# Kernel tuning notes

Measured on AMD Instinct MI355X. Metric: run time of the kernel, lower is better.

The kernel has to match this reference:

```python
import jax, jax.numpy as jnp
import numpy as np

KERNEL_SIZE = 5   # from __init__ default
SIGMA_S = 1.0     # spatial gaussian sigma (both axes)
SIGMA_R = 0.04    # range (color) gaussian sigma


def _space_kernel(k, sigma):
    # kornia-style 1D gaussian, normalized to sum 1, then outer product -> (k, k)
    x = jnp.arange(k, dtype=jnp.float32) - (k // 2)
    g = jnp.exp(-(x * x) / (2.0 * sigma * sigma))
    g = g / g.sum()
    return jnp.outer(g, g)


def setup_inputs() -> dict:
    key = jax.random.key(0)
    images = jax.random.uniform(key, (16, 512, 512, 3), dtype=jnp.float32)  # [B,H,W,3] in [0,1]
    return {"images": images}


def reference(images):
    k = KERNEL_SIZE
    pad = k // 2
    x = jnp.transpose(images, (0, 3, 1, 2))  # (B, C, H, W)
    B, C, H, W = x.shape
    xp = jnp.pad(x, ((0, 0), (0, 0), (pad, pad), (pad, pad)), mode="reflect")
    sk = _space_kernel(k, SIGMA_S).astype(x.dtype)
    inv2sr2 = 0.5 / (SIGMA_R * SIGMA_R)
    num = jnp.zeros_like(x)
    den = jnp.zeros((B, 1, H, W), dtype=x.dtype)
    # fused accumulation over the k*k window (fixed 25-tap loop, fully vectorized per tap)
    for dy in range(k):
        for dx in range(k):
            sh = xp[:, :, dy:dy + H, dx:dx + W]                  # shifted neighbor (B,C,H,W)
            d2 = jnp.sum((sh - x) ** 2, axis=1, keepdims=True)   # color distance^2 (B,1,H,W)
            w = sk[dy, dx] * jnp.exp(-inv2sr2 * d2)              # space * range weight
            num = num + w * sh
            den = den + w
    out = jnp.clip(num / den, 0.0, 1.0)
    return jnp.transpose(out, (0, 2, 3, 1))  # back to (B, H, W, C)
```

## Files before the change

kernel.cpp:

```cpp
#include <hip/hip_runtime.h>
#include <math.h>

#define IMG_H 512
#define IMG_W 512
#define CH    3
#define TILE_W 16
#define TILE_H 32
#define HALF  16
#define PAD   2
#define TP    20

typedef float v2f __attribute__((ext_vector_type(2)));
typedef float v4f __attribute__((ext_vector_type(4)));

#if __has_builtin(__builtin_amdgcn_exp2f)
#define EXP2(x) __builtin_amdgcn_exp2f(x)
#else
#define EXP2(x) exp2f(x)
#endif

#if __has_builtin(__builtin_amdgcn_rcpf)
#define RCP(x) __builtin_amdgcn_rcpf(x)
#else
#define RCP(x) (1.0f / (x))
#endif

__device__ __forceinline__ int reflect_idx(int i, int n) {
    i = (i < 0) ? -i : i;
    i = (i >= n) ? (2 * n - 2 - i) : i;
    return i;
}

__global__ __launch_bounds__(256)
void bilateral_kernel(const float* __restrict__ in, float* __restrict__ out) {
    __shared__ v4f planeP[TP][TP];
    __shared__ v4f planeQ[TP][TP];

    const float S = sqrtf(312.5f * 1.44269504088896f);

    const int b  = blockIdx.z;
    const int by = blockIdx.y * TILE_H;
    const int bx = blockIdx.x * TILE_W;
    const int tx = threadIdx.x;
    const int ty = threadIdx.y;
    const int tid = ty * TILE_W + tx;

    for (int i = tid; i < TP * TP; i += 256) {
        const int r  = i / TP;
        const int cc = i - r * TP;
        const int gyA = reflect_idx(by + r - PAD, IMG_H);
        const int gyB = reflect_idx(by + HALF + r - PAD, IMG_H);
        const int gx  = reflect_idx(bx + cc - PAD, IMG_W);
        const float* pA = in + ((size_t)(b * IMG_H + gyA) * IMG_W + gx) * CH;
        const float* pB = in + ((size_t)(b * IMG_H + gyB) * IMG_W + gx) * CH;
        const float a0 = pA[0] * S, a1 = pA[1] * S, a2 = pA[2] * S;
        const float e0 = pB[0] * S, e1 = pB[1] * S, e2 = pB[2] * S;
        const float wA = -fmaf(a0, a0, fmaf(a1, a1, a2 * a2));
        const float wB = -fmaf(e0, e0, fmaf(e1, e1, e2 * e2));
        planeP[r][cc] = (v4f){ a0, e0, a1, e1 };
        planeQ[r][cc] = (v4f){ a2, e2, wA, wB };
    }
    __syncthreads();

    const int rp = ((ty & 3) << 2) | (ty >> 2);

    const float CW[3] = { -4.1978935f, -2.0338538f, -1.3125121f };

    const v4f cP = planeP[rp + PAD][tx + PAD];
    const v4f cQ = planeQ[rp + PAD][tx + PAD];
    const v2f c2x = __builtin_shufflevector(cP, cP, 0, 1) + __builtin_shufflevector(cP, cP, 0, 1);
    const v2f c2y = __builtin_shufflevector(cP, cP, 2, 3) + __builtin_shufflevector(cP, cP, 2, 3);
    const v2f c2z = __builtin_shufflevector(cQ, cQ, 0, 1) + __builtin_shufflevector(cQ, cQ, 0, 1);
    const v2f cw  = __builtin_shufflevector(cQ, cQ, 2, 3);

    v2f base[3][3];
    #pragma unroll
    for (int iy = 0; iy < 3; ++iy)
        #pragma unroll
        for (int ix = 0; ix < 3; ++ix) {
            const float k = CW[iy] + CW[ix];
            base[iy][ix] = cw + (v2f){ k, k };
        }

    v2f nx = (v2f){0.f,0.f}, ny = (v2f){0.f,0.f};
    v2f nz = (v2f){0.f,0.f}, nd = (v2f){0.f,0.f};

    #pragma unroll
    for (int dy = 0; dy < 5; ++dy) {
        const int iy = (dy < 3) ? dy : 4 - dy;
        #pragma unroll
        for (int k = 0; k < 5; ++k) {
            const int ix = (k < 3) ? k : 4 - k;
            const v4f P = planeP[rp + dy][tx + k];
            const v4f Q = planeQ[rp + dy][tx + k];
            const v2f sx = __builtin_shufflevector(P, P, 0, 1);
            const v2f sy = __builtin_shufflevector(P, P, 2, 3);
            const v2f sz = __builtin_shufflevector(Q, Q, 0, 1);
            const v2f sw = __builtin_shufflevector(Q, Q, 2, 3);
            v2f t = sw + base[iy][ix];
            t = __builtin_elementwise_fma(sz, c2z, t);
            t = __builtin_elementwise_fma(sy, c2y, t);
            t = __builtin_elementwise_fma(sx, c2x, t);
            const v2f w = (v2f){ EXP2(t.x), EXP2(t.y) };
            nx = __builtin_elementwise_fma(w, sx, nx);
            ny = __builtin_elementwise_fma(w, sy, ny);
            nz = __builtin_elementwise_fma(w, sz, nz);
            nd = nd + w;
        }
    }

    const int xcol = bx + tx;
    {
        const float inv = RCP(nd.x * S);
        float* dst = out + ((size_t)(b * IMG_H + by + rp) * IMG_W + xcol) * CH;
        dst[0] = fminf(fmaxf(nx.x * inv, 0.0f), 1.0f);
        dst[1] = fminf(fmaxf(ny.x * inv, 0.0f), 1.0f);
        dst[2] = fminf(fmaxf(nz.x * inv, 0.0f), 1.0f);
    }
    {
        const float inv = RCP(nd.y * S);
        float* dst = out + ((size_t)(b * IMG_H + by + HALF + rp) * IMG_W + xcol) * CH;
        dst[0] = fminf(fmaxf(nx.y * inv, 0.0f), 1.0f);
        dst[1] = fminf(fmaxf(ny.y * inv, 0.0f), 1.0f);
        dst[2] = fminf(fmaxf(nz.y * inv, 0.0f), 1.0f);
    }
}

extern "C" void kernel_launch(void* const* d_in, const int* in_sizes, int n_in,
                              void* d_out, int out_size, void* d_ws, size_t ws_size,
                              hipStream_t stream) {
    const float* in = (const float*)d_in[0];
    float* out = (float*)d_out;
    const int B = in_sizes[0] / (IMG_H * IMG_W * CH);

    dim3 block(TILE_W, 16, 1);
    dim3 grid(IMG_W / TILE_W, IMG_H / TILE_H, B);
    bilateral_kernel<<<grid, block, 0, stream>>>(in, out);
}
```

Baseline: 38.24 us.

## Compute two vertically adjacent rows per thread to reuse shared-memory loads

Each thread now computes two adjacent output rows in each of the two packed half-tiles, so blocks shrink from 256 to 128 threads. The thread walks six stencil rows and applies every loaded tap to both outputs. This cuts LDS reads per output from 25 to 15 and drops the precomputed base table. In exchange there are more accumulator registers per thread, fewer waves per block to hide latency, and a heavier tile-load loop.

```diff
diff --git a/kernel.cpp b/kernel.cpp
--- a/kernel.cpp
+++ b/kernel.cpp
@@ -25,13 +25,16 @@
 #define RCP(x) (1.0f / (x))
 #endif
 
+#define LOV(a) __builtin_shufflevector(a, a, 0, 1)
+#define HIV(a) __builtin_shufflevector(a, a, 2, 3)
+
 __device__ __forceinline__ int reflect_idx(int i, int n) {
     i = (i < 0) ? -i : i;
     i = (i >= n) ? (2 * n - 2 - i) : i;
     return i;
 }
 
-__global__ __launch_bounds__(256)
+__global__ __launch_bounds__(128)
 void bilateral_kernel(const float* __restrict__ in, float* __restrict__ out) {
     __shared__ v4f planeP[TP][TP];
     __shared__ v4f planeQ[TP][TP];
@@ -45,7 +48,7 @@
     const int ty = threadIdx.y;
     const int tid = ty * TILE_W + tx;
 
-    for (int i = tid; i < TP * TP; i += 256) {
+    for (int i = tid; i < TP * TP; i += TILE_W * 8) {
         const int r  = i / TP;
         const int cc = i - r * TP;
         const int gyA = reflect_idx(by + r - PAD, IMG_H);
@@ -62,67 +65,80 @@
     }
     __syncthreads();
 
-    const int rp = ((ty & 3) << 2) | (ty >> 2);
+    const int r0 = ((ty & 3) << 2) | ((ty >> 2) << 1);
 
     const float CW[3] = { -4.1978935f, -2.0338538f, -1.3125121f };
 
-    const v4f cP = planeP[rp + PAD][tx + PAD];
-    const v4f cQ = planeQ[rp + PAD][tx + PAD];
-    const v2f c2x = __builtin_shufflevector(cP, cP, 0, 1) + __builtin_shufflevector(cP, cP, 0, 1);
-    const v2f c2y = __builtin_shufflevector(cP, cP, 2, 3) + __builtin_shufflevector(cP, cP, 2, 3);
-    const v2f c2z = __builtin_shufflevector(cQ, cQ, 0, 1) + __builtin_shufflevector(cQ, cQ, 0, 1);
-    const v2f cw  = __builtin_shufflevector(cQ, cQ, 2, 3);
+    const v4f* Pb = &planeP[r0][tx];
+    const v4f* Qb = &planeQ[r0][tx];
 
-    v2f base[3][3];
-    #pragma unroll
-    for (int iy = 0; iy < 3; ++iy)
-        #pragma unroll
-        for (int ix = 0; ix < 3; ++ix) {
-            const float k = CW[iy] + CW[ix];
-            base[iy][ix] = cw + (v2f){ k, k };
-        }
+    const v4f cP0 = Pb[2 * TP + 2], cQ0 = Qb[2 * TP + 2];
+    const v4f cP1 = Pb[3 * TP + 2], cQ1 = Qb[3 * TP + 2];
+    const v2f c2x0 = LOV(cP0) + LOV(cP0), c2y0 = HIV(cP0) + HIV(cP0);
+    const v2f c2z0 = LOV(cQ0) + LOV(cQ0), cw0  = HIV(cQ0);
+    const v2f c2x1 = LOV(cP1) + LOV(cP1), c2y1 = HIV(cP1) + HIV(cP1);
+    const v2f c2z1 = LOV(cQ1) + LOV(cQ1), cw1  = HIV(cQ1);
 
-    v2f nx = (v2f){0.f,0.f}, ny = (v2f){0.f,0.f};
-    v2f nz = (v2f){0.f,0.f}, nd = (v2f){0.f,0.f};
+    v2f nx0 = (v2f){0.f,0.f}, ny0 = nx0, nz0 = nx0, nd0 = nx0;
+    v2f nx1 = nx0, ny1 = nx0, nz1 = nx0, nd1 = nx0;
+
+#define TAP(c2x, c2y, c2z, cw, KC, nx, ny, nz, nd)                         \
+    do {                                                                   \
+        v2f t = __builtin_elementwise_fma(sz, c2z, sw);                    \
+        t = __builtin_elementwise_fma(sy, c2y, t);                         \
+        t = __builtin_elementwise_fma(sx, c2x, t);                         \
+        t = t + cw;                                                        \
+        t = t + (v2f){ KC, KC };                                           \
+        const v2f w = (v2f){ EXP2(t.x), EXP2(t.y) };                       \
+        nx = __builtin_elementwise_fma(w, sx, nx);                         \
+        ny = __builtin_elementwise_fma(w, sy, ny);                         \
+        nz = __builtin_elementwise_fma(w, sz, nz);                         \
+        nd = nd + w;                                                       \
+    } while (0)
 
     #pragma unroll
-    for (int dy = 0; dy < 5; ++dy) {
-        const int iy = (dy < 3) ? dy : 4 - dy;
+    for (int r = 0; r < 6; ++r) {
+        const int iy0 = (r < 3) ? r : 4 - r;
+        const int dy1 = r - 1;
+        const int iy1 = (dy1 < 3) ? dy1 : 4 - dy1;
         #pragma unroll
         for (int k = 0; k < 5; ++k) {
             const int ix = (k < 3) ? k : 4 - k;
-            const v4f P = planeP[rp + dy][tx + k];
-            const v4f Q = planeQ[rp + dy][tx + k];
-            const v2f sx = __builtin_shufflevector(P, P, 0, 1);
-            const v2f sy = __builtin_shufflevector(P, P, 2, 3);
-            const v2f sz = __builtin_shufflevector(Q, Q, 0, 1);
-            const v2f sw = __builtin_shufflevector(Q, Q, 2, 3);
-            v2f t = sw + base[iy][ix];
-            t = __builtin_elementwise_fma(sz, c2z, t);
-            t = __builtin_elementwise_fma(sy, c2y, t);
-            t = __builtin_elementwise_fma(sx, c2x, t);
-            const v2f w = (v2f){ EXP2(t.x), EXP2(t.y) };
-            nx = __builtin_elementwise_fma(w, sx, nx);
-            ny = __builtin_elementwise_fma(w, sy, ny);
-            nz = __builtin_elementwise_fma(w, sz, nz);
-            nd = nd + w;
+            const v4f P = Pb[r * TP + k];
+            const v4f Q = Qb[r * TP + k];
+            const v2f sx = LOV(P), sy = HIV(P);
+            const v2f sz = LOV(Q), sw = HIV(Q);
+            if (r <= 4) {
+                const float KC0 = CW[iy0] + CW[ix];
+                TAP(c2x0, c2y0, c2z0, cw0, KC0, nx0, ny0, nz0, nd0);
+            }
+            if (r >= 1) {
+                const float KC1 = CW[iy1] + CW[ix];
+                TAP(c2x1, c2y1, c2z1, cw1, KC1, nx1, ny1, nz1, nd1);
+            }
         }
     }
+#undef TAP
 
     const int xcol = bx + tx;
-    {
-        const float inv = RCP(nd.x * S);
-        float* dst = out + ((size_t)(b * IMG_H + by + rp) * IMG_W + xcol) * CH;
-        dst[0] = fminf(fmaxf(nx.x * inv, 0.0f), 1.0f);
-        dst[1] = fminf(fmaxf(ny.x * inv, 0.0f), 1.0f);
-        dst[2] = fminf(fmaxf(nz.x * inv, 0.0f), 1.0f);
-    }
-    {
-        const float inv = RCP(nd.y * S);
-        float* dst = out + ((size_t)(b * IMG_H + by + HALF + rp) * IMG_W + xcol) * CH;
-        dst[0] = fminf(fmaxf(nx.y * inv, 0.0f), 1.0f);
-        dst[1] = fminf(fmaxf(ny.y * inv, 0.0f), 1.0f);
-        dst[2] = fminf(fmaxf(nz.y * inv, 0.0f), 1.0f);
+    #pragma unroll
+    for (int j = 0; j < 2; ++j) {
+        const v2f nx = j ? nx1 : nx0, ny = j ? ny1 : ny0;
+        const v2f nz = j ? nz1 : nz0, nd = j ? nd1 : nd0;
+        {
+            const float inv = RCP(nd.x * S);
+            float* dst = out + ((size_t)(b * IMG_H + by + r0 + j) * IMG_W + xcol) * CH;
+            dst[0] = fminf(fmaxf(nx.x * inv, 0.0f), 1.0f);
+            dst[1] = fminf(fmaxf(ny.x * inv, 0.0f), 1.0f);
+            dst[2] = fminf(fmaxf(nz.x * inv, 0.0f), 1.0f);
+        }
+        {
+            const float inv = RCP(nd.y * S);
+            float* dst = out + ((size_t)(b * IMG_H + by + HALF + r0 + j) * IMG_W + xcol) * CH;
+            dst[0] = fminf(fmaxf(nx.y * inv, 0.0f), 1.0f);
+            dst[1] = fminf(fmaxf(ny.y * inv, 0.0f), 1.0f);
+            dst[2] = fminf(fmaxf(nz.y * inv, 0.0f), 1.0f);
+        }
     }
 }
 
@@ -133,7 +149,7 @@
     float* out = (float*)d_out;
     const int B = in_sizes[0] / (IMG_H * IMG_W * CH);
 
-    dim3 block(TILE_W, 16, 1);
+    dim3 block(TILE_W, 8, 1);
     dim3 grid(IMG_W / TILE_W, IMG_H / TILE_H, B);
     bilateral_kernel<<<grid, block, 0, stream>>>(in, out);
 }
```

New measurement: 67.31 us. 1.76x slower.

## Switch bilateral accumulation to packed fp16 and process four row groups per thread

Applied to the files above, without the earlier changes.

Stores the shared-memory tile as packed half2 values holding four row groups (AB and CD pairs) and computes color distance, exp2 weights and accumulations with packed half-precision instructions. Each thread now handles four output rows instead of two, and the block tile height doubles to 64. The aim is to double arithmetic throughput per instruction and cut the number of blocks. The cost is fp16 accuracy loss in the weights and sums (exp2 of arguments near -450·d2, accumulation of 25 terms), which may exceed tolerance. Each block also does more global loads per thread during tile fill.

```diff
diff --git a/kernel.cpp b/kernel.cpp
--- a/kernel.cpp
+++ b/kernel.cpp
@@ -1,23 +1,15 @@
 #include <hip/hip_runtime.h>
+#include <hip/hip_fp16.h>
 #include <math.h>
 
 #define IMG_H 512
 #define IMG_W 512
 #define CH    3
 #define TILE_W 16
-#define TILE_H 32
-#define HALF  16
+#define TILE_H 64
+#define QTR   16
 #define PAD   2
 #define TP    20
-
-typedef float v2f __attribute__((ext_vector_type(2)));
-typedef float v4f __attribute__((ext_vector_type(4)));
-
-#if __has_builtin(__builtin_amdgcn_exp2f)
-#define EXP2(x) __builtin_amdgcn_exp2f(x)
-#else
-#define EXP2(x) exp2f(x)
-#endif
 
 #if __has_builtin(__builtin_amdgcn_rcpf)
 #define RCP(x) __builtin_amdgcn_rcpf(x)
@@ -31,12 +23,17 @@
     return i;
 }
 
+__device__ __forceinline__ __half2 bch(unsigned int u) {
+    return __builtin_bit_cast(__half2, u);
+}
+__device__ __forceinline__ unsigned int hcb(__half2 h) {
+    return __builtin_bit_cast(unsigned int, h);
+}
+
 __global__ __launch_bounds__(256)
 void bilateral_kernel(const float* __restrict__ in, float* __restrict__ out) {
-    __shared__ v4f planeP[TP][TP];
-    __shared__ v4f planeQ[TP][TP];
-
-    const float S = sqrtf(312.5f * 1.44269504088896f);
+    __shared__ uint4 H4[TP][TP];
+    __shared__ uint2 H2[TP][TP];
 
     const int b  = blockIdx.z;
     const int by = blockIdx.y * TILE_H;
@@ -48,42 +45,46 @@
     for (int i = tid; i < TP * TP; i += 256) {
         const int r  = i / TP;
         const int cc = i - r * TP;
+        const int gx  = reflect_idx(bx + cc - PAD, IMG_W);
         const int gyA = reflect_idx(by + r - PAD, IMG_H);
-        const int gyB = reflect_idx(by + HALF + r - PAD, IMG_H);
-        const int gx  = reflect_idx(bx + cc - PAD, IMG_W);
+        const int gyB = reflect_idx(by + QTR + r - PAD, IMG_H);
+        const int gyC = reflect_idx(by + 2 * QTR + r - PAD, IMG_H);
+        const int gyD = reflect_idx(by + 3 * QTR + r - PAD, IMG_H);
         const float* pA = in + ((size_t)(b * IMG_H + gyA) * IMG_W + gx) * CH;
         const float* pB = in + ((size_t)(b * IMG_H + gyB) * IMG_W + gx) * CH;
-        const float a0 = pA[0] * S, a1 = pA[1] * S, a2 = pA[2] * S;
-        const float e0 = pB[0] * S, e1 = pB[1] * S, e2 = pB[2] * S;
-        const float wA = -fmaf(a0, a0, fmaf(a1, a1, a2 * a2));
-        const float wB = -fmaf(e0, e0, fmaf(e1, e1, e2 * e2));
-        planeP[r][cc] = (v4f){ a0, e0, a1, e1 };
-        planeQ[r][cc] = (v4f){ a2, e2, wA, wB };
+        const float* pC = in + ((size_t)(b * IMG_H + gyC) * IMG_W + gx) * CH;
+        const float* pD = in + ((size_t)(b * IMG_H + gyD) * IMG_W + gx) * CH;
+        uint4 h4;
+        uint2 h2;
+        h4.x = hcb(__floats2half2_rn(pA[0], pB[0]));
+        h4.y = hcb(__floats2half2_rn(pC[0], pD[0]));
+        h4.z = hcb(__floats2half2_rn(pA[1], pB[1]));
+        h4.w = hcb(__floats2half2_rn(pC[1], pD[1]));
+        h2.x = hcb(__floats2half2_rn(pA[2], pB[2]));
+        h2.y = hcb(__floats2half2_rn(pC[2], pD[2]));
+        H4[r][cc] = h4;
+        H2[r][cc] = h2;
     }
     __syncthreads();
 
     const int rp = ((ty & 3) << 2) | (ty >> 2);
 
-    const float CW[3] = { -4.1978935f, -2.0338538f, -1.3125121f };
+    const __half2 K2 = __float2half2_rn(-450.8422f);
+    const __half2 B2[3][3] = {
+        { __float2half2_rn(-8.395800f), __float2half2_rn(-6.231757f), __float2half2_rn(-5.510409f) },
+        { __float2half2_rn(-6.231757f), __float2half2_rn(-4.067714f), __float2half2_rn(-3.346367f) },
+        { __float2half2_rn(-5.510409f), __float2half2_rn(-3.346367f), __float2half2_rn(-2.625024f) },
+    };
 
-    const v4f cP = planeP[rp + PAD][tx + PAD];
-    const v4f cQ = planeQ[rp + PAD][tx + PAD];
-    const v2f c2x = __builtin_shufflevector(cP, cP, 0, 1) + __builtin_shufflevector(cP, cP, 0, 1);
-    const v2f c2y = __builtin_shufflevector(cP, cP, 2, 3) + __builtin_shufflevector(cP, cP, 2, 3);
-    const v2f c2z = __builtin_shufflevector(cQ, cQ, 0, 1) + __builtin_shufflevector(cQ, cQ, 0, 1);
-    const v2f cw  = __builtin_shufflevector(cQ, cQ, 2, 3);
+    const uint4 cP = H4[rp + PAD][tx + PAD];
+    const uint2 cQ = H2[rp + PAD][tx + PAD];
+    const __half2 cxAB = bch(cP.x), cxCD = bch(cP.y);
+    const __half2 cyAB = bch(cP.z), cyCD = bch(cP.w);
+    const __half2 czAB = bch(cQ.x), czCD = bch(cQ.y);
 
-    v2f base[3][3];
-    #pragma unroll
-    for (int iy = 0; iy < 3; ++iy)
-        #pragma unroll
-        for (int ix = 0; ix < 3; ++ix) {
-            const float k = CW[iy] + CW[ix];
-            base[iy][ix] = cw + (v2f){ k, k };
-        }
-
-    v2f nx = (v2f){0.f,0.f}, ny = (v2f){0.f,0.f};
-    v2f nz = (v2f){0.f,0.f}, nd = (v2f){0.f,0.f};
+    const __half2 z2 = __float2half2_rn(0.0f);
+    __half2 nxAB = z2, nyAB = z2, nzAB = z2, ndAB = z2;
+    __half2 nxCD = z2, nyCD = z2, nzCD = z2, ndCD = z2;
 
     #pragma unroll
     for (int dy = 0; dy < 5; ++dy) {
@@ -91,38 +92,52 @@
         #pragma unroll
         for (int k = 0; k < 5; ++k) {
             const int ix = (k < 3) ? k : 4 - k;
-            const v4f P = planeP[rp + dy][tx + k];
-            const v4f Q = planeQ[rp + dy][tx + k];
-            const v2f sx = __builtin_shufflevector(P, P, 0, 1);
-            const v2f sy = __builtin_shufflevector(P, P, 2, 3);
-            const v2f sz = __builtin_shufflevector(Q, Q, 0, 1);
-            const v2f sw = __builtin_shufflevector(Q, Q, 2, 3);
-            v2f t = sw + base[iy][ix];
-            t = __builtin_elementwise_fma(sz, c2z, t);
-            t = __builtin_elementwise_fma(sy, c2y, t);
-            t = __builtin_elementwise_fma(sx, c2x, t);
-            const v2f w = (v2f){ EXP2(t.x), EXP2(t.y) };
-            nx = __builtin_elementwise_fma(w, sx, nx);
-            ny = __builtin_elementwise_fma(w, sy, ny);
-            nz = __builtin_elementwise_fma(w, sz, nz);
-            nd = nd + w;
+            const uint4 P = H4[rp + dy][tx + k];
+            const uint2 Q = H2[rp + dy][tx + k];
+            const __half2 sxAB = bch(P.x), sxCD = bch(P.y);
+            const __half2 syAB = bch(P.z), syCD = bch(P.w);
+            const __half2 szAB = bch(Q.x), szCD = bch(Q.y);
+            {
+                const __half2 dx = __hsub2(sxAB, cxAB);
+                const __half2 dyh = __hsub2(syAB, cyAB);
+                const __half2 dz = __hsub2(szAB, czAB);
+                const __half2 d2 = __hfma2(dx, dx, __hfma2(dyh, dyh, __hmul2(dz, dz)));
+                const __half2 arg = __hfma2(d2, K2, B2[iy][ix]);
+                const __half2 w = h2exp2(arg);
+                nxAB = __hfma2(w, sxAB, nxAB);
+                nyAB = __hfma2(w, syAB, nyAB);
+                nzAB = __hfma2(w, szAB, nzAB);
+                ndAB = __hadd2(ndAB, w);
+            }
+            {
+                const __half2 dx = __hsub2(sxCD, cxCD);
+                const __half2 dyh = __hsub2(syCD, cyCD);
+                const __half2 dz = __hsub2(szCD, czCD);
+                const __half2 d2 = __hfma2(dx, dx, __hfma2(dyh, dyh, __hmul2(dz, dz)));
+                const __half2 arg = __hfma2(d2, K2, B2[iy][ix]);
+                const __half2 w = h2exp2(arg);
+                nxCD = __hfma2(w, sxCD, nxCD);
+                nyCD = __hfma2(w, syCD, nyCD);
+                nzCD = __hfma2(w, szCD, nzCD);
+                ndCD = __hadd2(ndCD, w);
+            }
         }
     }
 
     const int xcol = bx + tx;
-    {
-        const float inv = RCP(nd.x * S);
-        float* dst = out + ((size_t)(b * IMG_H + by + rp) * IMG_W + xcol) * CH;
-        dst[0] = fminf(fmaxf(nx.x * inv, 0.0f), 1.0f);
-        dst[1] = fminf(fmaxf(ny.x * inv, 0.0f), 1.0f);
-        dst[2] = fminf(fmaxf(nz.x * inv, 0.0f), 1.0f);
-    }
-    {
-        const float inv = RCP(nd.y * S);
-        float* dst = out + ((size_t)(b * IMG_H + by + HALF + rp) * IMG_W + xcol) * CH;
-        dst[0] = fminf(fmaxf(nx.y * inv, 0.0f), 1.0f);
-        dst[1] = fminf(fmaxf(ny.y * inv, 0.0f), 1.0f);
-        dst[2] = fminf(fmaxf(nz.y * inv, 0.0f), 1.0f);
+    #pragma unroll
+    for (int q = 0; q < 4; ++q) {
+        float n0, n1, n2, den;
+        if (q == 0) { n0 = __low2float(nxAB);  n1 = __low2float(nyAB);  n2 = __low2float(nzAB);  den = __low2float(ndAB); }
+        else if (q == 1) { n0 = __high2float(nxAB); n1 = __high2float(nyAB); n2 = __high2float(nzAB); den = __high2float(ndAB); }
+        else if (q == 2) { n0 = __low2float(nxCD);  n1 = __low2float(nyCD);  n2 = __low2float(nzCD);  den = __low2float(ndCD); }
+        else { n0 = __high2float(nxCD); n1 = __high2float(nyCD); n2 = __high2float(nzCD); den = __high2float(ndCD); }
+        const float inv = RCP(den);
+        const int y = by + q * QTR + rp;
+        float* dst = out + ((size_t)(b * IMG_H + y) * IMG_W + xcol) * CH;
+        dst[0] = fminf(fmaxf(n0 * inv, 0.0f), 1.0f);
+        dst[1] = fminf(fmaxf(n1 * inv, 0.0f), 1.0f);
+        dst[2] = fminf(fmaxf(n2 * inv, 0.0f), 1.0f);
     }
 }
 
```

New measurement: 39.22 us. 2.6% more time.
